# Performance work log

Measured on AMD Instinct MI355X. Metric: run time of the kernel, lower is better.

Reference implementation:

```python
import jax, jax.numpy as jnp
import numpy as np

B, H = 2048, 1024
P_DROP = 0.6


def setup_inputs() -> dict:
    key = jax.random.key(0)
    ks = jax.random.split(key, 17)
    stdv = 1.0 / np.sqrt(H)
    u = lambda k, shape: jax.random.uniform(k, shape, jnp.float32, -stdv, stdv)
    inp = {
        'input': jax.random.normal(ks[0], (B, H), jnp.float32),
        'hidden': jax.random.normal(ks[1], (B, H), jnp.float32),
        'pre_cell': jax.random.normal(ks[2], (B, H), jnp.float32),
        # weights are (hidden_size, input_size) and used as input @ W (requires H == input_size)
        'w_i': u(ks[3], (H, H)), 'w_f': u(ks[4], (H, H)),
        'w_o': u(ks[5], (H, H)), 'w_c': u(ks[6], (H, H)),
        'u_i': u(ks[7], (H, H)), 'u_f': u(ks[8], (H, H)),
        'u_o': u(ks[9], (H, H)), 'u_c': u(ks[10], (H, H)),
        'bias1': u(ks[11], (H,)), 'bias2': u(ks[12], (H,)),
        'bias3': u(ks[13], (H,)), 'bias4': u(ks[14], (H,)),
    }
    # F.dropout(training=True) mask, pre-scaled by 1/(1-p); shape matches h_t [B,1,H]
    keep = jax.random.bernoulli(ks[15], 1.0 - P_DROP, (B, 1, H))
    inp['drop_mask'] = keep.astype(jnp.float32) / (1.0 - P_DROP)
    return inp


def reference(input, hidden, pre_cell, w_i, w_f, w_o, w_c, u_i, u_f, u_o, u_c,
              bias1, bias2, bias3, bias4, drop_mask):
    # Fuse the 8 small GEMMs into 2 big ones: gate order (f, i, o, c)
    Wx = jnp.concatenate([w_f, w_i, w_o, w_c], axis=1)   # [H, 4H]
    Wh = jnp.concatenate([u_f, u_i, u_o, u_c], axis=1)   # [H, 4H]
    b = jnp.concatenate([bias1, bias2, bias3, bias4])    # [4H]
    gates = input @ Wx + hidden @ Wh + b                 # [B, 4H]
    f_t, i_t, o_t, g_t = jnp.split(gates, 4, axis=1)
    f_t = jax.nn.sigmoid(f_t)
    i_t = jax.nn.sigmoid(i_t)
    o_t = jax.nn.sigmoid(o_t)
    g_t = jnp.tanh(g_t)
    c_t = pre_cell * f_t + i_t * g_t                     # [B, H]
    h_t = o_t * jnp.tanh(c_t)                            # [B, H]
    h_t = h_t[:, None, :] * drop_mask                    # dropout (training=True)
    c_t = c_t[:, None, :]
    return h_t, c_t
```

## Files before the change

kernel.cpp:

```cpp
#include <hip/hip_runtime.h>
#include <hip/hip_bf16.h>
#include <cstdint>

#define B_DIM 2048
#define H_DIM 1024
#define K_DIM 2048
#define N_DIM 4096

typedef unsigned short u16;
typedef __attribute__((ext_vector_type(8))) short bf16x8;
typedef __attribute__((ext_vector_type(8))) unsigned short u16x8;
typedef __attribute__((ext_vector_type(4))) float f32x4;

__device__ __forceinline__ u16 f2bf(float f) {
    unsigned int u = __float_as_uint(f);
    u += 0x7FFFu + ((u >> 16) & 1u);
    return (u16)(u >> 16);
}

__device__ __forceinline__ float sigmoid_f(float x) {
    return 1.0f / (1.0f + __expf(-x));
}

__device__ __forceinline__ float tanh_f(float x) {
    float e = __expf(2.0f * x);
    return 1.0f - 2.0f / (e + 1.0f);
}

__device__ __forceinline__ void async16(const u16* g, u16* l) {
    __builtin_amdgcn_global_load_lds(
        (const __attribute__((address_space(1))) unsigned int*)g,
        (__attribute__((address_space(3))) unsigned int*)l,
        16, 0, 0);
}

__global__ __launch_bounds__(256) void pack_all(
    const float* __restrict__ input, const float* __restrict__ hidden,
    const float* __restrict__ w_f, const float* __restrict__ w_i,
    const float* __restrict__ w_o, const float* __restrict__ w_c,
    const float* __restrict__ u_f, const float* __restrict__ u_i,
    const float* __restrict__ u_o, const float* __restrict__ u_c,
    const float* __restrict__ b1, const float* __restrict__ b2,
    const float* __restrict__ b3, const float* __restrict__ b4,
    u16* __restrict__ A, u16* __restrict__ Bt, float* __restrict__ bias_il) {
    __shared__ float tile[32][65];
    const int blk = blockIdx.x;
    const int t = threadIdx.x;

    if (blk < 4096) {
        int idx = (blk * 256 + t) * 4;
        int m = idx >> 11;
        int k = idx & (K_DIM - 1);
        const float* src = (k < H_DIM) ? (input + (size_t)m * H_DIM + k)
                                       : (hidden + (size_t)m * H_DIM + (k - H_DIM));
        float4 v = *(const float4*)src;
        ushort4 o;
        o.x = f2bf(v.x); o.y = f2bf(v.y); o.z = f2bf(v.z); o.w = f2bf(v.w);
        *(ushort4*)(A + idx) = o;
    } else if (blk < 8192) {
        int b2i = blk - 4096;
        int z = b2i >> 9;
        int rem = b2i & 511;
        int hx = rem & 31;
        int ky = rem >> 5;
        const float* M;
        switch (z) {
            case 0: M = w_f; break;
            case 1: M = w_i; break;
            case 2: M = w_o; break;
            case 3: M = w_c; break;
            case 4: M = u_f; break;
            case 5: M = u_i; break;
            case 6: M = u_o; break;
            default: M = u_c; break;
        }
        const int g = z & 3;
        const int half = z >> 2;
        const int h0 = hx * 32;
        const int k0 = ky * 64;
#pragma unroll
        for (int it = 0; it < 2; it++) {
            int kl = (t >> 3) + it * 32;
            int hl = (t & 7) * 4;
            float4 v = *(const float4*)(M + (size_t)(k0 + kl) * H_DIM + h0 + hl);
            tile[hl + 0][kl] = v.x;
            tile[hl + 1][kl] = v.y;
            tile[hl + 2][kl] = v.z;
            tile[hl + 3][kl] = v.w;
        }
        __syncthreads();
        int hl = t >> 3;
        int ko = (t & 7) * 8;
        u16x8 o;
#pragma unroll
        for (int q = 0; q < 8; q++) o[q] = f2bf(tile[hl][ko + q]);
        size_t n = 4 * (size_t)(h0 + hl) + g;
        *(u16x8*)(Bt + n * K_DIM + half * H_DIM + k0 + ko) = o;
    } else {
        int idx = (blk - 8192) * 256 + t;
        int h = idx >> 2, g = idx & 3;
        const float* b = (g == 0) ? b1 : (g == 1) ? b2 : (g == 2) ? b3 : b4;
        bias_il[idx] = b[h];
    }
}

#define BM 128
#define BN 128
#define BK 128
#define SL (64 * 32)

__global__ __launch_bounds__(256, 2) void gemm_fused(
    const u16* __restrict__ A, const u16* __restrict__ Bt,
    const float* __restrict__ bias_il, const float* __restrict__ pre_cell,
    const float* __restrict__ mask, float* __restrict__ out) {
    __shared__ char smem[65536];
    float* et = (float*)smem;

    const int t = threadIdx.x;
    const int w = t >> 6, l = t & 63;
    const int m0 = blockIdx.y * BM;
    const int n0 = blockIdx.x * BN;
    const int wr = w >> 1;
    const int wc = w & 1;
    const int lrow = l & 15;
    const int quad = l >> 4;

    const int sr = w * 16 + (l >> 2);
    const int sc = (l & 3) * 8;
    const u16* Ag0 = A + (size_t)(m0 + sr) * K_DIM + sc;
    const u16* Ag1 = Ag0 + (size_t)64 * K_DIM;
    const u16* Bg0 = Bt + (size_t)(n0 + sr) * K_DIM + sc;
    const u16* Bg1 = Bg0 + (size_t)64 * K_DIM;
    const int soff = sr * 32 + sc;

    const int foA = (wr * 64 + lrow) * 32 + quad * 8;
    const int foB = (wc * 64 + lrow) * 32 + quad * 8;

    f32x4 acc[4][4];
#pragma unroll
    for (int j = 0; j < 4; j++) {
        float bv = bias_il[n0 + wc * 64 + j * 16 + lrow];
#pragma unroll
        for (int i = 0; i < 4; i++) acc[i][j] = (f32x4){bv, bv, bv, bv};
    }

#define COMPUTE(Asb, Bsb)                                                   \
    {                                                                       \
        bf16x8 af[4], bf[4];                                                \
        _Pragma("unroll") for (int i = 0; i < 4; i++)                       \
            af[i] = *(const bf16x8*)((Asb) + foA + i * 16 * 32);            \
        _Pragma("unroll") for (int j = 0; j < 4; j++)                       \
            bf[j] = *(const bf16x8*)((Bsb) + foB + j * 16 * 32);            \
        _Pragma("unroll") for (int i = 0; i < 4; i++)                       \
            _Pragma("unroll") for (int j = 0; j < 4; j++)                   \
                acc[i][j] = __builtin_amdgcn_mfma_f32_16x16x32_bf16(        \
                    af[i], bf[j], acc[i][j], 0, 0, 0);                      \
    }

    for (int k0 = 0; k0 < K_DIM; k0 += BK) {
        __syncthreads();
#pragma unroll
        for (int s = 0; s < 4; s++) {
            u16* Asl = (u16*)(smem + s * 8192);
            u16* Bsl = (u16*)(smem + 32768 + s * 8192);
            async16(Ag0 + k0 + s * 32, Asl + soff);
            async16(Ag1 + k0 + s * 32, Asl + soff + SL);
            async16(Bg0 + k0 + s * 32, Bsl + soff);
            async16(Bg1 + k0 + s * 32, Bsl + soff + SL);
        }
        __syncthreads();
#pragma unroll
        for (int s = 0; s < 4; s++) {
            const u16* Asl = (const u16*)(smem + s * 8192);
            const u16* Bsl = (const u16*)(smem + 32768 + s * 8192);
            COMPUTE(Asl, Bsl);
        }
    }
#undef COMPUTE

    const int row = t >> 1;
    const int half = t & 1;
    const size_t orow = (size_t)(m0 + row) * H_DIM;

    float4 pc[4], mk[4];
#pragma unroll
    for (int j = 0; j < 4; j++) {
        const int hg0 = (n0 >> 2) + half * 16 + j * 4;
        pc[j] = *(const float4*)(pre_cell + orow + hg0);
        mk[j] = *(const float4*)(mask + orow + hg0);
    }

#pragma unroll
    for (int j = 0; j < 4; j++) {
        __syncthreads();
#pragma unroll
        for (int i = 0; i < 4; i++)
#pragma unroll
            for (int r = 0; r < 4; r++)
                et[(wr * 64 + i * 16 + quad * 4 + r) * 33 + wc * 16 + lrow] =
                    acc[i][j][r];
        __syncthreads();
        const int hg0 = (n0 >> 2) + half * 16 + j * 4;
        const float* ep = et + row * 33 + half * 16;
        const float* ppc = (const float*)&pc[j];
        const float* pmk = (const float*)&mk[j];
        float4 oh, oc;
        float* poh = (float*)&oh;
        float* poc = (float*)&oc;
#pragma unroll
        for (int q = 0; q < 4; q++) {
            float fv = sigmoid_f(ep[4 * q + 0]);
            float iv = sigmoid_f(ep[4 * q + 1]);
            float ov = sigmoid_f(ep[4 * q + 2]);
            float gv = tanh_f(ep[4 * q + 3]);
            float cv = ppc[q] * fv + iv * gv;
            poc[q] = cv;
            poh[q] = ov * tanh_f(cv) * pmk[q];
        }
        *(float4*)(out + orow + hg0) = oh;
        *(float4*)(out + (size_t)B_DIM * H_DIM + orow + hg0) = oc;
    }
}

extern "C" void kernel_launch(void* const* d_in, const int* in_sizes, int n_in,
                              void* d_out, int out_size, void* d_ws, size_t ws_size,
                              hipStream_t stream) {
    const float* input    = (const float*)d_in[0];
    const float* hidden   = (const float*)d_in[1];
    const float* pre_cell = (const float*)d_in[2];
    const float* w_i = (const float*)d_in[3];
    const float* w_f = (const float*)d_in[4];
    const float* w_o = (const float*)d_in[5];
    const float* w_c = (const float*)d_in[6];
    const float* u_i = (const float*)d_in[7];
    const float* u_f = (const float*)d_in[8];
    const float* u_o = (const float*)d_in[9];
    const float* u_c = (const float*)d_in[10];
    const float* b1  = (const float*)d_in[11];
    const float* b2  = (const float*)d_in[12];
    const float* b3  = (const float*)d_in[13];
    const float* b4  = (const float*)d_in[14];
    const float* mask = (const float*)d_in[15];
    float* out = (float*)d_out;

    char* ws = (char*)d_ws;
    u16*   A       = (u16*)ws;
    u16*   Bt      = (u16*)(ws + (size_t)8 * 1024 * 1024);
    float* bias_il = (float*)(ws + (size_t)24 * 1024 * 1024);

    pack_all<<<dim3(4096 + 4096 + 16), dim3(256), 0, stream>>>(
        input, hidden, w_f, w_i, w_o, w_c, u_f, u_i, u_o, u_c,
        b1, b2, b3, b4, A, Bt, bias_il);
    gemm_fused<<<dim3(N_DIM / BN, B_DIM / BM), dim3(256), 0, stream>>>(
        A, Bt, bias_il, pre_cell, mask, out);
}
```

Baseline: 164.5 us.

## Pipeline GEMM K-loop with 4-stage async LDS ring and swizzled layout

```diff
diff --git a/kernel.cpp b/kernel.cpp
--- a/kernel.cpp
+++ b/kernel.cpp
@@ -106,8 +106,6 @@
 
 #define BM 128
 #define BN 128
-#define BK 128
-#define SL (64 * 32)
 
 __global__ __launch_bounds__(256, 2) void gemm_fused(
     const u16* __restrict__ A, const u16* __restrict__ Bt,
@@ -125,16 +123,16 @@
     const int lrow = l & 15;
     const int quad = l >> 4;
 
-    const int sr = w * 16 + (l >> 2);
-    const int sc = (l & 3) * 8;
-    const u16* Ag0 = A + (size_t)(m0 + sr) * K_DIM + sc;
-    const u16* Ag1 = Ag0 + (size_t)64 * K_DIM;
-    const u16* Bg0 = Bt + (size_t)(n0 + sr) * K_DIM + sc;
-    const u16* Bg1 = Bg0 + (size_t)64 * K_DIM;
-    const int soff = sr * 32 + sc;
-
-    const int foA = (wr * 64 + lrow) * 32 + quad * 8;
-    const int foB = (wc * 64 + lrow) * 32 + quad * 8;
+    const int srow = t >> 2;
+    const int skswz = ((t & 3) * 8) ^ ((srow & 6) << 2);
+    const u16* AgS0 = A + (size_t)(m0 + srow) * K_DIM + skswz;
+    const u16* AgS1 = AgS0 + (size_t)64 * K_DIM;
+    const u16* BgS0 = Bt + (size_t)(n0 + srow) * K_DIM + skswz;
+    const u16* BgS1 = BgS0 + (size_t)64 * K_DIM;
+
+    const int swzf = (quad * 8) ^ ((lrow & 6) << 2);
+    const int foA = (wr * 64 + lrow) * 32 + swzf;
+    const int foB = (wc * 64 + lrow) * 32 + swzf;
 
     f32x4 acc[4][4];
 #pragma unroll
@@ -144,39 +142,59 @@
         for (int i = 0; i < 4; i++) acc[i][j] = (f32x4){bv, bv, bv, bv};
     }
 
-#define COMPUTE(Asb, Bsb)                                                   \
+#pragma unroll
+    for (int p = 0; p < 3; ++p) {
+        u16* As_ = (u16*)(smem + p * 16384);
+        u16* Bs_ = As_ + 4096;
+        const int ko_ = p * 32;
+        async16(AgS0 + ko_, As_ + t * 8);
+        async16(AgS1 + ko_, As_ + 2048 + t * 8);
+        async16(BgS0 + ko_, Bs_ + t * 8);
+        async16(BgS1 + ko_, Bs_ + 2048 + t * 8);
+    }
+
+#define KSTEP(kt, DO_STAGE, VM)                                             \
     {                                                                       \
+        if (DO_STAGE) {                                                     \
+            u16* As_ = (u16*)(smem + (((kt) + 3) & 3) * 16384);             \
+            u16* Bs_ = As_ + 4096;                                          \
+            const int ko_ = ((kt) + 3) * 32;                                \
+            async16(AgS0 + ko_, As_ + t * 8);                               \
+            async16(AgS1 + ko_, As_ + 2048 + t * 8);                        \
+            async16(BgS0 + ko_, Bs_ + t * 8);                               \
+            async16(BgS1 + ko_, Bs_ + 2048 + t * 8);                        \
+        }                                                                   \
+        asm volatile("s_waitcnt vmcnt(" #VM ")" ::: "memory");              \
+        __builtin_amdgcn_s_barrier();                                       \
+        asm volatile("" ::: "memory");                                      \
+        const u16* As = (const u16*)(smem + ((kt) & 3) * 16384);            \
+        const u16* Bs = As + 4096;                                          \
         bf16x8 af[4], bf[4];                                                \
         _Pragma("unroll") for (int i = 0; i < 4; i++)                       \
-            af[i] = *(const bf16x8*)((Asb) + foA + i * 16 * 32);            \
+            af[i] = *(const bf16x8*)(As + foA + i * 512);                   \
         _Pragma("unroll") for (int j = 0; j < 4; j++)                       \
-            bf[j] = *(const bf16x8*)((Bsb) + foB + j * 16 * 32);            \
+            bf[j] = *(const bf16x8*)(Bs + foB + j * 512);                   \
+        __builtin_amdgcn_s_setprio(1);                                      \
         _Pragma("unroll") for (int i = 0; i < 4; i++)                       \
             _Pragma("unroll") for (int j = 0; j < 4; j++)                   \
                 acc[i][j] = __builtin_amdgcn_mfma_f32_16x16x32_bf16(        \
                     af[i], bf[j], acc[i][j], 0, 0, 0);                      \
-    }
-
-    for (int k0 = 0; k0 < K_DIM; k0 += BK) {
-        __syncthreads();
-#pragma unroll
-        for (int s = 0; s < 4; s++) {
-            u16* Asl = (u16*)(smem + s * 8192);
-            u16* Bsl = (u16*)(smem + 32768 + s * 8192);
-            async16(Ag0 + k0 + s * 32, Asl + soff);
-            async16(Ag1 + k0 + s * 32, Asl + soff + SL);
-            async16(Bg0 + k0 + s * 32, Bsl + soff);
-            async16(Bg1 + k0 + s * 32, Bsl + soff + SL);
-        }
-        __syncthreads();
-#pragma unroll
-        for (int s = 0; s < 4; s++) {
-            const u16* Asl = (const u16*)(smem + s * 8192);
-            const u16* Bsl = (const u16*)(smem + 32768 + s * 8192);
-            COMPUTE(Asl, Bsl);
-        }
-    }
-#undef COMPUTE
+        __builtin_amdgcn_s_setprio(0);                                      \
+        asm volatile("" ::: "memory");                                      \
+        __builtin_amdgcn_s_barrier();                                       \
+    }
+
+    for (int kt = 0; kt < 60; kt += 4) {
+        KSTEP(kt + 0, true, 12);
+        KSTEP(kt + 1, true, 12);
+        KSTEP(kt + 2, true, 12);
+        KSTEP(kt + 3, true, 12);
+    }
+    KSTEP(60, true, 12);
+    KSTEP(61, false, 8);
+    KSTEP(62, false, 4);
+    KSTEP(63, false, 0);
+#undef KSTEP
 
     const int row = t >> 1;
     const int half = t & 1;
```

Result: slower. 169.6 us (+3.1%).

## Pre-tile B into MFMA fragment layout and XOR-swizzle LDS tiles

Applied to the files above, without the earlier changes.

```diff
diff --git a/kernel.cpp b/kernel.cpp
--- a/kernel.cpp
+++ b/kernel.cpp
@@ -42,7 +42,7 @@
     const float* __restrict__ u_o, const float* __restrict__ u_c,
     const float* __restrict__ b1, const float* __restrict__ b2,
     const float* __restrict__ b3, const float* __restrict__ b4,
-    u16* __restrict__ A, u16* __restrict__ Bt, float* __restrict__ bias_il) {
+    u16* __restrict__ A, u16* __restrict__ Bf, float* __restrict__ bias_il) {
     __shared__ float tile[32][65];
     const int blk = blockIdx.x;
     const int t = threadIdx.x;
@@ -95,7 +95,12 @@
 #pragma unroll
         for (int q = 0; q < 8; q++) o[q] = f2bf(tile[hl][ko + q]);
         size_t n = 4 * (size_t)(h0 + hl) + g;
-        *(u16x8*)(Bt + n * K_DIM + half * H_DIM + k0 + ko) = o;
+        int kg = half * H_DIM + k0 + ko;
+        size_t ntile = n >> 4;
+        int nrow = (int)(n & 15);
+        int kt = kg >> 5;
+        int k8 = (kg >> 3) & 3;
+        *(u16x8*)(Bf + ((ntile * 64 + kt) * 64 + (k8 * 16 + nrow)) * 8) = o;
     } else {
         int idx = (blk - 8192) * 256 + t;
         int h = idx >> 2, g = idx & 3;
@@ -110,7 +115,7 @@
 #define SL (64 * 32)
 
 __global__ __launch_bounds__(256, 2) void gemm_fused(
-    const u16* __restrict__ A, const u16* __restrict__ Bt,
+    const u16* __restrict__ A, const u16* __restrict__ Bf,
     const float* __restrict__ bias_il, const float* __restrict__ pre_cell,
     const float* __restrict__ mask, float* __restrict__ out) {
     __shared__ char smem[65536];
@@ -127,14 +132,18 @@
 
     const int sr = w * 16 + (l >> 2);
     const int sc = (l & 3) * 8;
-    const u16* Ag0 = A + (size_t)(m0 + sr) * K_DIM + sc;
+    const int skswz = sc ^ ((sr & 6) << 2);
+    const u16* Ag0 = A + (size_t)(m0 + sr) * K_DIM + skswz;
     const u16* Ag1 = Ag0 + (size_t)64 * K_DIM;
-    const u16* Bg0 = Bt + (size_t)(n0 + sr) * K_DIM + sc;
-    const u16* Bg1 = Bg0 + (size_t)64 * K_DIM;
+    const int k8s = (skswz >> 3) & 3;
+    const u16* Bg0 = Bf + ((size_t)(n0 >> 4) + (sr >> 4)) * 32768
+                        + (size_t)k8s * 128 + (size_t)(sr & 15) * 8;
+    const u16* Bg1 = Bg0 + 131072;
     const int soff = sr * 32 + sc;
 
-    const int foA = (wr * 64 + lrow) * 32 + quad * 8;
-    const int foB = (wc * 64 + lrow) * 32 + quad * 8;
+    const int swzf = (quad * 8) ^ ((lrow & 6) << 2);
+    const int foA = (wr * 64 + lrow) * 32 + swzf;
+    const int foB = (wc * 64 + lrow) * 32 + swzf;
 
     f32x4 acc[4][4];
 #pragma unroll
@@ -148,9 +157,9 @@
     {                                                                       \
         bf16x8 af[4], bf[4];                                                \
         _Pragma("unroll") for (int i = 0; i < 4; i++)                       \
-            af[i] = *(const bf16x8*)((Asb) + foA + i * 16 * 32);            \
+            af[i] = *(const bf16x8*)((Asb) + foA + i * 512);                \
         _Pragma("unroll") for (int j = 0; j < 4; j++)                       \
-            bf[j] = *(const bf16x8*)((Bsb) + foB + j * 16 * 32);            \
+            bf[j] = *(const bf16x8*)((Bsb) + foB + j * 512);                \
         _Pragma("unroll") for (int i = 0; i < 4; i++)                       \
             _Pragma("unroll") for (int j = 0; j < 4; j++)                   \
                 acc[i][j] = __builtin_amdgcn_mfma_f32_16x16x32_bf16(        \
@@ -159,14 +168,15 @@
 
     for (int k0 = 0; k0 < K_DIM; k0 += BK) {
         __syncthreads();
+        const int kb = (k0 >> 5) * 512;
 #pragma unroll
         for (int s = 0; s < 4; s++) {
             u16* Asl = (u16*)(smem + s * 8192);
             u16* Bsl = (u16*)(smem + 32768 + s * 8192);
             async16(Ag0 + k0 + s * 32, Asl + soff);
             async16(Ag1 + k0 + s * 32, Asl + soff + SL);
-            async16(Bg0 + k0 + s * 32, Bsl + soff);
-            async16(Bg1 + k0 + s * 32, Bsl + soff + SL);
+            async16(Bg0 + kb + s * 512, Bsl + soff);
+            async16(Bg1 + kb + s * 512, Bsl + soff + SL);
         }
         __syncthreads();
 #pragma unroll
@@ -245,12 +255,12 @@
 
     char* ws = (char*)d_ws;
     u16*   A       = (u16*)ws;
-    u16*   Bt      = (u16*)(ws + (size_t)8 * 1024 * 1024);
+    u16*   Bf      = (u16*)(ws + (size_t)8 * 1024 * 1024);
     float* bias_il = (float*)(ws + (size_t)24 * 1024 * 1024);
 
     pack_all<<<dim3(4096 + 4096 + 16), dim3(256), 0, stream>>>(
         input, hidden, w_f, w_i, w_o, w_c, u_f, u_i, u_o, u_c,
-        b1, b2, b3, b4, A, Bt, bias_il);
+        b1, b2, b3, b4, A, Bf, bias_il);
     gemm_fused<<<dim3(N_DIM / BN, B_DIM / BM), dim3(256), 0, stream>>>(
-        A, Bt, bias_il, pre_cell, mask, out);
-}
+        A, Bf, bias_il, pre_cell, mask, out);
+}
```

Result: slower. 176.8 us (+7.4%).
